# Performance work log

Measured on AMD Instinct MI355X. Metric: run time of the kernel, lower is better.

The kernel has to match this reference:

```python
import jax, jax.numpy as jnp
import numpy as np

B, T, INP, HID, ACT = 64, 1000, 64, 512, 2

def setup_inputs() -> dict:
    key = jax.random.key(0)
    k1, k2, k3, k4, k5 = jax.random.split(key, 5)
    s_hh = (6.0 / (HID + HID)) ** 0.5  # xavier_uniform bounds
    s_ih = (6.0 / (INP + HID)) ** 0.5
    s_fc = (6.0 / (HID + ACT)) ** 0.5
    return {
        "inp": jax.random.normal(k1, (B, T, INP), dtype=jnp.float32),
        "hn": jax.random.normal(k2, (1, B, HID), dtype=jnp.float32),
        "W_hh": jax.random.uniform(k3, (HID, HID), jnp.float32, -s_hh, s_hh),
        "W_ih": jax.random.uniform(k4, (INP, HID), jnp.float32, -s_ih, s_ih),
        "W_fc": jax.random.uniform(k5, (HID, ACT), jnp.float32, -s_fc, s_fc),
        "b_fc": jnp.zeros((ACT,), dtype=jnp.float32),
    }

def reference(inp, hn, W_hh, W_ih, W_fc, b_fc):
    # Precompute input projections for all timesteps in one big GEMM: [B,T,H]
    inp_proj = jnp.einsum("bti,ih->bth", inp, W_ih)
    h0 = hn[0]  # [B, H]

    def step(h, x_t):
        h_next = jax.nn.sigmoid(h @ W_hh + x_t)
        return h_next, h_next

    # scan over time: xs must be time-major
    _, hs = jax.lax.scan(step, h0, jnp.swapaxes(inp_proj, 0, 1))
    rnn_out = jnp.swapaxes(hs, 0, 1)  # [B, T, H]
    hn_last = rnn_out[:, -1, :][None]  # [1, B, H]
    out = jax.nn.sigmoid(rnn_out @ W_fc + b_fc)  # [B, T, ACT]
    return (out, hn_last, rnn_out)
```

## Files before the change

### kernel.cpp

```cpp
#include <hip/hip_runtime.h>
#include <hip/hip_bf16.h>
#include <stdint.h>
#include <math.h>

#define B   64
#define T   1000
#define INP 64
#define HID 512
#define ACT 2

#define NSLICE 4
#define MROWS  2
#define NGROUP (B / MROWS)
#define NBLOCKS (NGROUP * NSLICE)
#define COLS   (HID / NSLICE)
#define HLPAD  544

typedef __attribute__((ext_vector_type(8))) short short8;
typedef __attribute__((ext_vector_type(4))) float floatx4;

__global__ __launch_bounds__(256) void init_kernel(
    const float* __restrict__ hn, uint32_t* __restrict__ h_ex) {
  const int i = blockIdx.x * 256 + threadIdx.x;
  __hip_bfloat16 b = __float2bfloat16(hn[i]);
  const uint32_t hb = *reinterpret_cast<unsigned short*>(&b);
  h_ex[(size_t)B * HID + i] = (hb << 16) | 0u;
  h_ex[i] = 0xFFFEu;
}

__global__ __launch_bounds__(256) void xproj_kernel(
    const float* __restrict__ inp, const float* __restrict__ W_ih,
    float* __restrict__ rnn) {
  __shared__ float xin[16 * INP];
  const int tid = threadIdx.x;
  const long r0 = (long)blockIdx.x * 16;

  const float4* inp4 = (const float4*)(inp + r0 * INP);
  ((float4*)xin)[tid] = inp4[tid];
  __syncthreads();

  const int j = tid, j2 = tid + 256;
  float acc0[16], acc1[16];
#pragma unroll
  for (int r = 0; r < 16; ++r) { acc0[r] = 0.f; acc1[r] = 0.f; }

  for (int i = 0; i < INP; ++i) {
    const float w0 = W_ih[i * HID + j];
    const float w1 = W_ih[i * HID + j2];
#pragma unroll
    for (int r = 0; r < 16; ++r) {
      const float x = xin[r * INP + i];
      acc0[r] = fmaf(x, w0, acc0[r]);
      acc1[r] = fmaf(x, w1, acc1[r]);
    }
  }
#pragma unroll
  for (int r = 0; r < 16; ++r) {
    rnn[(r0 + r) * HID + j]  = acc0[r];
    rnn[(r0 + r) * HID + j2] = acc1[r];
  }
}

__global__ __launch_bounds__(512) void rnn_mfma(
    const float* __restrict__ W_hh, float* __restrict__ rnn,
    float* __restrict__ hn_out, uint32_t* __restrict__ h_ex) {
  __shared__ __align__(16) unsigned short hl[2][MROWS][HLPAD];

  const int tid  = threadIdx.x;
  const int lane = tid & 63;
  const int w    = tid >> 6;
  const int g    = blockIdx.x & (NGROUP - 1);
  const int s    = blockIdx.x >> 5;
  const int r0   = g * MROWS;
  const int n_base = s * COLS + w * 16;

  const int lm = lane & 15;
  const int lq = lane >> 4;
  const int cc = n_base + lm;

  short8 bfrag[16];
#pragma unroll
  for (int kt = 0; kt < 16; ++kt) {
    short8 f;
#pragma unroll
    for (int i = 0; i < 8; ++i) {
      const int k = kt * 32 + lq * 8 + i;
      __hip_bfloat16 hb = __float2bfloat16(W_hh[k * HID + cc]);
      f[i] = *reinterpret_cast<short*>(&hb);
    }
    bfrag[kt] = f;
  }

  const int  arow   = lm & 1;
  const bool remote = ((tid >> 7) != s);
  const bool prod   = (lq == 0);

  long ro0 = ((long)r0 * T + 0) * HID + cc;
  long ro1 = ((long)(r0 + 1) * T + 0) * HID + cc;
  float xp0 = 0.f, xp1 = 0.f;
  if (prod) { xp0 = rnn[ro0]; xp1 = rnn[ro1]; }

  for (int t = 0; t < T; ++t) {
    const int p = (t + 1) & 1;

    if (t == 0 || remote) {
      uint32_t* src = h_ex + (size_t)p * B * HID + (size_t)r0 * HID + tid;
      const uint32_t want = (uint32_t)t & 0xFFFFu;
      uint32_t v0, v1;
      int guard = 0;
      for (;;) {
        v0 = __hip_atomic_load(src, __ATOMIC_RELAXED,
                               __HIP_MEMORY_SCOPE_AGENT);
        v1 = __hip_atomic_load(src + HID, __ATOMIC_RELAXED,
                               __HIP_MEMORY_SCOPE_AGENT);
        if ((((v0 ^ want) | (v1 ^ want)) & 0xFFFFu) == 0) break;
        if (++guard > (1 << 20)) break;
      }
      hl[p][0][tid] = (unsigned short)(v0 >> 16);
      hl[p][1][tid] = (unsigned short)(v1 >> 16);
    }
    __syncthreads();

    float nxp0 = 0.f, nxp1 = 0.f;
    long nro0 = ro0, nro1 = ro1;
    if (prod && t + 1 < T) {
      nro0 = ro0 + HID; nro1 = ro1 + HID;
      nxp0 = rnn[nro0]; nxp1 = rnn[nro1];
    }

    floatx4 c0 = {0.f, 0.f, 0.f, 0.f}, c1 = c0, c2 = c0, c3 = c0;
    const unsigned short* ap = &hl[p][arow][lq * 8];
#pragma unroll
    for (int kt = 0; kt < 16; kt += 4) {
      short8 a0 = *(const short8*)(ap + (kt + 0) * 32);
      short8 a1 = *(const short8*)(ap + (kt + 1) * 32);
      short8 a2 = *(const short8*)(ap + (kt + 2) * 32);
      short8 a3 = *(const short8*)(ap + (kt + 3) * 32);
      c0 = __builtin_amdgcn_mfma_f32_16x16x32_bf16(a0, bfrag[kt + 0], c0, 0, 0, 0);
      c1 = __builtin_amdgcn_mfma_f32_16x16x32_bf16(a1, bfrag[kt + 1], c1, 0, 0, 0);
      c2 = __builtin_amdgcn_mfma_f32_16x16x32_bf16(a2, bfrag[kt + 2], c2, 0, 0, 0);
      c3 = __builtin_amdgcn_mfma_f32_16x16x32_bf16(a3, bfrag[kt + 3], c3, 0, 0, 0);
    }

    if (prod) {
      const float z0 = c0[0] + c1[0] + c2[0] + c3[0] + xp0;
      const float z1 = c0[1] + c1[1] + c2[1] + c3[1] + xp1;
      const float h0 = 1.f / (1.f + __expf(-z0));
      const float h1 = 1.f / (1.f + __expf(-z1));
      __hip_bfloat16 b0 = __float2bfloat16(h0);
      __hip_bfloat16 b1 = __float2bfloat16(h1);
      const unsigned short u0 = *reinterpret_cast<unsigned short*>(&b0);
      const unsigned short u1 = *reinterpret_cast<unsigned short*>(&b1);

      const uint32_t tag = (uint32_t)(t + 1) & 0xFFFFu;
      uint32_t* dst = h_ex + (size_t)(t & 1) * B * HID + (size_t)r0 * HID + cc;
      __hip_atomic_store(dst, ((uint32_t)u0 << 16) | tag,
                         __ATOMIC_RELAXED, __HIP_MEMORY_SCOPE_AGENT);
      __hip_atomic_store(dst + HID, ((uint32_t)u1 << 16) | tag,
                         __ATOMIC_RELAXED, __HIP_MEMORY_SCOPE_AGENT);

      hl[t & 1][0][cc] = u0;
      hl[t & 1][1][cc] = u1;

      rnn[ro0] = h0;
      rnn[ro1] = h1;
      if (t == T - 1) {
        hn_out[r0 * HID + cc]       = h0;
        hn_out[(r0 + 1) * HID + cc] = h1;
      }
      xp0 = nxp0; xp1 = nxp1; ro0 = nro0; ro1 = nro1;
    }
  }
}

__global__ __launch_bounds__(256) void fc_kernel(
    const float* __restrict__ rnn, const float* __restrict__ W_fc,
    const float* __restrict__ b_fc, float* __restrict__ out) {
  const int lane = threadIdx.x & 63;
  const int wid  = threadIdx.x >> 6;
  const long row = (long)blockIdx.x * 4 + wid;

  const float4* __restrict__ hrow = (const float4*)(rnn + row * HID);
  const float4* __restrict__ Wfc4 = (const float4*)W_fc;

  float a0 = 0.f, a1 = 0.f;
#pragma unroll
  for (int u = 0; u < 2; ++u) {
    const float4 hv = hrow[lane * 2 + u];
    const int j0 = lane * 8 + u * 4;
    const float4 wA = Wfc4[(j0 >> 1)];
    const float4 wB = Wfc4[(j0 >> 1) + 1];
    a0 += hv.x * wA.x + hv.y * wA.z + hv.z * wB.x + hv.w * wB.z;
    a1 += hv.x * wA.y + hv.y * wA.w + hv.z * wB.y + hv.w * wB.w;
  }
#pragma unroll
  for (int off = 32; off > 0; off >>= 1) {
    a0 += __shfl_down(a0, off, 64);
    a1 += __shfl_down(a1, off, 64);
  }
  if (lane == 0) {
    out[row * 2 + 0] = 1.f / (1.f + __expf(-(a0 + b_fc[0])));
    out[row * 2 + 1] = 1.f / (1.f + __expf(-(a1 + b_fc[1])));
  }
}

extern "C" void kernel_launch(void* const* d_in, const int* in_sizes, int n_in,
                              void* d_out, int out_size, void* d_ws,
                              size_t ws_size, hipStream_t stream) {
  const float* inp  = (const float*)d_in[0];
  const float* hn   = (const float*)d_in[1];
  const float* W_hh = (const float*)d_in[2];
  const float* W_ih = (const float*)d_in[3];
  const float* W_fc = (const float*)d_in[4];
  const float* b_fc = (const float*)d_in[5];

  float* out    = (float*)d_out;
  float* hn_out = out + (long)B * T * ACT;
  float* rnn    = hn_out + (long)B * HID;

  uint32_t* h_ex = (uint32_t*)d_ws;

  hipLaunchKernelGGL(init_kernel, dim3((B * HID) / 256), dim3(256), 0, stream,
                     hn, h_ex);
  hipLaunchKernelGGL(xproj_kernel, dim3((B * T) / 16), dim3(256), 0, stream,
                     inp, W_ih, rnn);
  hipLaunchKernelGGL(rnn_mfma, dim3(NBLOCKS), dim3(512), 0, stream,
                     W_hh, rnn, hn_out, h_ex);
  hipLaunchKernelGGL(fc_kernel, dim3((B * T) / 4), dim3(256), 0, stream,
                     rnn, W_fc, b_fc, out);
}
```

Measured before the change: 1.661 ms.

## Pack hidden-state exchange into 64-bit words and poll via L2-scoped inline asm

Repacks the cross-block hidden-state exchange buffer so each 64-bit word carries both batch rows with their step tags. Polling and publishing now use single dwordx2 loads and stores, replacing two agent-scope atomics per thread. A fast path uses inline-asm global loads with the sc0 bit and plain stores, meant to cut per-step synchronisation latency on the serial T loop. A second buffer written with agent-scope atomics serves as a fallback if the fast path times out, at the cost of a duplicated store every step and reliance on cache-coherence behaviour the inline asm may not guarantee.

```diff
diff --git a/kernel.cpp b/kernel.cpp
--- a/kernel.cpp
+++ b/kernel.cpp
@@ -16,16 +16,39 @@
 #define COLS   (HID / NSLICE)
 #define HLPAD  544
 
+#define FAST_GUARD 1024
+
 typedef __attribute__((ext_vector_type(8))) short short8;
 typedef __attribute__((ext_vector_type(4))) float floatx4;
 
+__device__ __forceinline__ uint64_t l2_load64(const uint64_t* p) {
+  uint64_t v;
+  asm volatile("global_load_dwordx2 %0, %1, off sc0\n\t"
+               "s_waitcnt vmcnt(0)"
+               : "=v"(v) : "v"(p) : "memory");
+  return v;
+}
+__device__ __forceinline__ void l2_store64(uint64_t* p, uint64_t v) {
+  asm volatile("global_store_dwordx2 %0, %1, off"
+               :: "v"(p), "v"(v) : "memory");
+}
+
 __global__ __launch_bounds__(256) void init_kernel(
-    const float* __restrict__ hn, uint32_t* __restrict__ h_ex) {
-  const int i = blockIdx.x * 256 + threadIdx.x;
-  __hip_bfloat16 b = __float2bfloat16(hn[i]);
-  const uint32_t hb = *reinterpret_cast<unsigned short*>(&b);
-  h_ex[(size_t)B * HID + i] = (hb << 16) | 0u;
-  h_ex[i] = 0xFFFEu;
+    const float* __restrict__ hn, uint64_t* __restrict__ h_fast,
+    uint64_t* __restrict__ h_safe) {
+  const int i   = blockIdx.x * 256 + threadIdx.x;
+  const int g   = i >> 9;
+  const int col = i & (HID - 1);
+  __hip_bfloat16 b0 = __float2bfloat16(hn[(2 * g) * HID + col]);
+  __hip_bfloat16 b1 = __float2bfloat16(hn[(2 * g + 1) * HID + col]);
+  const uint32_t w0 = ((uint32_t)*reinterpret_cast<unsigned short*>(&b0)) << 16;
+  const uint32_t w1 = ((uint32_t)*reinterpret_cast<unsigned short*>(&b1)) << 16;
+  const uint64_t v  = (uint64_t)w0 | ((uint64_t)w1 << 32);
+  const size_t p1 = (size_t)NGROUP * HID + i;
+  h_fast[p1] = v;
+  h_safe[p1] = v;
+  h_fast[i] = 0x0000FFFE0000FFFEull;
+  h_safe[i] = 0x0000FFFE0000FFFEull;
 }
 
 __global__ __launch_bounds__(256) void xproj_kernel(
@@ -63,7 +86,8 @@
 
 __global__ __launch_bounds__(512) void rnn_mfma(
     const float* __restrict__ W_hh, float* __restrict__ rnn,
-    float* __restrict__ hn_out, uint32_t* __restrict__ h_ex) {
+    float* __restrict__ hn_out, uint64_t* __restrict__ h_fast,
+    uint64_t* __restrict__ h_safe) {
   __shared__ __align__(16) unsigned short hl[2][MROWS][HLPAD];
 
   const int tid  = threadIdx.x;
@@ -100,24 +124,34 @@
   float xp0 = 0.f, xp1 = 0.f;
   if (prod) { xp0 = rnn[ro0]; xp1 = rnn[ro1]; }
 
+  int fastmode = 1;
+
   for (int t = 0; t < T; ++t) {
     const int p = (t + 1) & 1;
 
     if (t == 0 || remote) {
-      uint32_t* src = h_ex + (size_t)p * B * HID + (size_t)r0 * HID + tid;
-      const uint32_t want = (uint32_t)t & 0xFFFFu;
-      uint32_t v0, v1;
-      int guard = 0;
-      for (;;) {
-        v0 = __hip_atomic_load(src, __ATOMIC_RELAXED,
-                               __HIP_MEMORY_SCOPE_AGENT);
-        v1 = __hip_atomic_load(src + HID, __ATOMIC_RELAXED,
-                               __HIP_MEMORY_SCOPE_AGENT);
-        if ((((v0 ^ want) | (v1 ^ want)) & 0xFFFFu) == 0) break;
-        if (++guard > (1 << 20)) break;
+      const size_t idx = ((size_t)p * NGROUP + g) * HID + tid;
+      const uint64_t want = (uint64_t)(t & 0xFFFF) * 0x0000000100000001ull;
+      uint64_t v = 0;
+      if (fastmode) {
+        int ok = 0;
+        for (int it = 0; it < FAST_GUARD; ++it) {
+          v = l2_load64(h_fast + idx);
+          if (((v ^ want) & 0x0000FFFF0000FFFFull) == 0) { ok = 1; break; }
+        }
+        if (!ok) fastmode = 0;
       }
-      hl[p][0][tid] = (unsigned short)(v0 >> 16);
-      hl[p][1][tid] = (unsigned short)(v1 >> 16);
+      if (!fastmode) {
+        int guard = 0;
+        for (;;) {
+          v = __hip_atomic_load(h_safe + idx, __ATOMIC_RELAXED,
+                                __HIP_MEMORY_SCOPE_AGENT);
+          if (((v ^ want) & 0x0000FFFF0000FFFFull) == 0) break;
+          if (++guard > (1 << 20)) break;
+        }
+      }
+      hl[p][0][tid] = (unsigned short)((uint32_t)v >> 16);
+      hl[p][1][tid] = (unsigned short)((uint32_t)(v >> 32) >> 16);
     }
     __syncthreads();
 
@@ -153,11 +187,13 @@
       const unsigned short u1 = *reinterpret_cast<unsigned short*>(&b1);
 
       const uint32_t tag = (uint32_t)(t + 1) & 0xFFFFu;
-      uint32_t* dst = h_ex + (size_t)(t & 1) * B * HID + (size_t)r0 * HID + cc;
-      __hip_atomic_store(dst, ((uint32_t)u0 << 16) | tag,
-                         __ATOMIC_RELAXED, __HIP_MEMORY_SCOPE_AGENT);
-      __hip_atomic_store(dst + HID, ((uint32_t)u1 << 16) | tag,
-                         __ATOMIC_RELAXED, __HIP_MEMORY_SCOPE_AGENT);
+      const uint64_t word =
+          (uint64_t)(((uint32_t)u0 << 16) | tag) |
+          ((uint64_t)(((uint32_t)u1 << 16) | tag) << 32);
+      const size_t didx = ((size_t)(t & 1) * NGROUP + g) * HID + cc;
+      l2_store64(h_fast + didx, word);
+      __hip_atomic_store(h_safe + didx, word, __ATOMIC_RELAXED,
+                         __HIP_MEMORY_SCOPE_AGENT);
 
       hl[t & 1][0][cc] = u0;
       hl[t & 1][1][cc] = u1;
@@ -218,14 +254,17 @@
   float* hn_out = out + (long)B * T * ACT;
   float* rnn    = hn_out + (long)B * HID;
 
-  uint32_t* h_ex = (uint32_t*)d_ws;
-
-  hipLaunchKernelGGL(init_kernel, dim3((B * HID) / 256), dim3(256), 0, stream,
-                     hn, h_ex);
+  uint64_t* h_fast = (uint64_t*)d_ws;
+  const size_t HCNT = (size_t)2 * NGROUP * HID;
+  uint64_t* h_safe =
+      (ws_size >= 2 * HCNT * sizeof(uint64_t)) ? (h_fast + HCNT) : h_fast;
+
+  hipLaunchKernelGGL(init_kernel, dim3((NGROUP * HID) / 256), dim3(256), 0,
+                     stream, hn, h_fast, h_safe);
   hipLaunchKernelGGL(xproj_kernel, dim3((B * T) / 16), dim3(256), 0, stream,
                      inp, W_ih, rnn);
   hipLaunchKernelGGL(rnn_mfma, dim3(NBLOCKS), dim3(512), 0, stream,
-                     W_hh, rnn, hn_out, h_ex);
+                     W_hh, rnn, hn_out, h_fast, h_safe);
   hipLaunchKernelGGL(fc_kernel, dim3((B * T) / 4), dim3(256), 0, stream,
                      rnn, W_fc, b_fc, out);
 }
```

New measurement: 1.794 ms. 8.0% more time.
